# Performance work log

Hardware: AMD Instinct MI355X
Metric: run time of the kernel (lower is better)

## Reference

```python
import jax, jax.numpy as jnp
import numpy as np

NUM_LAYERS = 3
CHANNELS = 8
IN_CHANNELS = 8
MASK_OUT_STRIDE = 4
WEIGHT_NUMS = [(IN_CHANNELS + 2) * CHANNELS, CHANNELS * CHANNELS, CHANNELS]
BIAS_NUMS = [CHANNELS, CHANNELS, 1]
NUM_GEN_PARAMS = sum(WEIGHT_NUMS) + sum(BIAS_NUMS)  # 169
SOI = np.array([64.0, 128.0, 256.0, 512.0, 1024.0], dtype=np.float32)


def compute_locations(h, w, stride):
    # FCOS grid point centers, (H*W, 2) in (x, y) order
    shifts_x = jnp.arange(w, dtype=jnp.float32) * stride + stride // 2
    shifts_y = jnp.arange(h, dtype=jnp.float32) * stride + stride // 2
    ys, xs = jnp.meshgrid(shifts_y, shifts_x, indexing='ij')
    return jnp.stack([xs.reshape(-1), ys.reshape(-1)], axis=1)


def parse_dynamic_params(params):
    # params: (n_inst, 169) -> per-layer weights (n, cout, cin) and biases (n, cout)
    n = params.shape[0]
    split_pts = np.cumsum(WEIGHT_NUMS + BIAS_NUMS)[:-1].tolist()
    splits = jnp.split(params, split_pts, axis=1)
    ws, bs = [], []
    for l in range(NUM_LAYERS):
        cout = CHANNELS if l < NUM_LAYERS - 1 else 1
        ws.append(splits[l].reshape(n, cout, -1))
        bs.append(splits[NUM_LAYERS + l].reshape(n, cout))
    return ws, bs


def aligned_bilinear(x, factor):
    # Faithful port of AdelaiDet aligned_bilinear (replicate pad + align_corners=True bilinear).
    if factor == 1:
        return x
    n, c, h, w = x.shape
    xp = jnp.pad(x, ((0, 0), (0, 0), (0, 1), (0, 1)), mode='edge')  # (n,c,h+1,w+1)
    oh, ow = factor * h + 1, factor * w + 1
    # align_corners=True with oh = factor*h+1 over h+1 samples -> exact coords i/factor
    ys = jnp.arange(oh, dtype=x.dtype) / factor
    xs = jnp.arange(ow, dtype=x.dtype) / factor
    y0 = jnp.floor(ys).astype(jnp.int32)
    y1 = jnp.minimum(y0 + 1, h)
    x0 = jnp.floor(xs).astype(jnp.int32)
    x1 = jnp.minimum(x0 + 1, w)
    wy = (ys - y0.astype(x.dtype))[None, None, :, None]
    wx = (xs - x0.astype(x.dtype))[None, None, None, :]
    rows = xp[:, :, y0, :] * (1 - wy) + xp[:, :, y1, :] * wy
    out = rows[:, :, :, x0] * (1 - wx) + rows[:, :, :, x1] * wx
    pad = factor // 2
    out = jnp.pad(out, ((0, 0), (0, 0), (pad, 0), (pad, 0)), mode='edge')
    return out[:, :, :oh - 1, :ow - 1]  # (n, c, factor*h, factor*w)


def dynamic_head(x, params):
    # x: (n_inst, cin, HW); per-instance 1x1 convs == batched tiny GEMMs
    ws, bs = parse_dynamic_params(params)
    h = x
    for i, (w, b) in enumerate(zip(ws, bs)):
        h = jnp.einsum('noi,nip->nop', w, h) + b[:, :, None]
        if i < NUM_LAYERS - 1:
            h = jax.nn.relu(h)
    return h  # (n_inst, 1, HW)


def setup_inputs() -> dict:
    key = jax.random.key(0)
    k = jax.random.split(key, 6)
    N, H, W, n_inst = 2, 200, 200, 128
    return {
        'mask_feats': jax.random.normal(k[0], (N, IN_CHANNELS, H, W), jnp.float32),
        'mask_head_params': jax.random.normal(k[1], (n_inst, NUM_GEN_PARAMS), jnp.float32) * 0.1,
        'boundary_head_params': jax.random.normal(k[2], (n_inst, NUM_GEN_PARAMS), jnp.float32) * 0.1,
        'instance_locations': jax.random.uniform(k[3], (n_inst, 2), jnp.float32) * 1600.0,
        'im_inds': jax.random.randint(k[4], (n_inst,), 0, N),
        'fpn_levels': jax.random.randint(k[5], (n_inst,), 0, 5),
        'mask_feat_stride': 8,
    }


def reference(mask_feats, mask_head_params, boundary_head_params, instance_locations, im_inds, fpn_levels, mask_feat_stride):
    N, C, H, W = mask_feats.shape
    n_inst = mask_head_params.shape[0]
    locs = compute_locations(H, W, mask_feat_stride)                 # (HW, 2)
    rel = instance_locations[:, None, :] - locs[None, :, :]          # (n, HW, 2)
    rel = jnp.transpose(rel, (0, 2, 1))                              # (n, 2, HW)
    soi = jnp.asarray(SOI)[fpn_levels]                               # (n,)
    rel = (rel / soi[:, None, None]).astype(mask_feats.dtype)
    feats = mask_feats[im_inds].reshape(n_inst, C, H * W)            # per-instance gather
    x = jnp.concatenate([rel, feats], axis=1)                        # (n, C+2, HW)
    factor = mask_feat_stride // MASK_OUT_STRIDE
    m = aligned_bilinear(dynamic_head(x, mask_head_params).reshape(n_inst, 1, H, W), factor)
    bd = aligned_bilinear(dynamic_head(x, boundary_head_params).reshape(n_inst, 1, H, W), factor)
    return jax.nn.sigmoid(m), jax.nn.sigmoid(bd)
```

## Files before the change

### kernel.cpp

```cpp
#include <hip/hip_runtime.h>


#define BLOCK 256
#define Hh 200
#define Ww 200
#define NP 169
#define TH 25
#define MAXR 14
#define OW 400
#define OH 400

typedef float f32x4 __attribute__((ext_vector_type(4)));
typedef float f32x2 __attribute__((ext_vector_type(2)));
typedef _Float16 f16x4 __attribute__((ext_vector_type(4)));

__device__ __forceinline__ f32x2 splat2(float v) { f32x2 r; r.x = v; r.y = v; return r; }
__device__ __forceinline__ f32x2 pkfma(f32x2 a, f32x2 b, f32x2 c) {
    return __builtin_elementwise_fma(a, b, c);
}

__global__ __launch_bounds__(BLOCK, 4) void dmh_fused(
    const float* __restrict__ mask_feats,
    const float* __restrict__ mparams,
    const float* __restrict__ bparams,
    const float* __restrict__ ilocs,
    const int*   __restrict__ im_inds,
    const int*   __restrict__ fpn_levels,
    const int*   __restrict__ stride_p,
    float* __restrict__ out,
    int n_inst)
{
    __shared__ __align__(16) float s_par[2 * 192];
    __shared__ __align__(16) _Float16 s_m[2][MAXR][Ww];

    const int tid  = threadIdx.x;
    const int tile = blockIdx.x;
    const int inst = blockIdx.y;

    for (int j = tid; j < 2 * NP; j += BLOCK) {
        const int head = (j < NP) ? 0 : 1;
        const int k = j - head * NP;
        const float v = head ? bparams[inst * NP + k] : mparams[inst * NP + k];
        int dst;
        if      (k < 80)  dst = (k / 10) * 12 + (k % 10);
        else if (k < 144) dst = 96 + (k - 80);
        else if (k < 152) dst = 160 + (k - 144);
        else if (k < 160) dst = 168 + (k - 152);
        else if (k < 168) dst = 176 + (k - 160);
        else              dst = 184;
        s_par[head * 192 + dst] = v;
    }

    const int   s    = stride_p[0];
    const int   half = s >> 1;
    const int   im   = im_inds[inst];
    const int   lvl  = fpn_levels[inst];
    const float inv_soi = 1.0f / (float)(64 << lvl);
    const float ixl = ilocs[inst * 2 + 0];
    const float iyl = ilocs[inst * 2 + 1];

    const int i0 = tile * TH;
    const int r_begin = ((i0 > 0) ? (i0 - 1) : 0) >> 1;
    int r_end = ((i0 + TH - 2) >> 1) + 1;
    if (r_end > Hh - 1) r_end = Hh - 1;
    const int nrows = r_end - r_begin + 1;

    __syncthreads();

    const int npx = nrows * Ww;
    const float* fbase = mask_feats + (size_t)im * 8 * Hh * Ww;

    for (int g = tid * 4; g < npx; g += BLOCK * 4) {
        asm volatile("" ::: "memory");

        const int lr = g / Ww;
        const int c  = g - lr * Ww;
        const int r  = r_begin + lr;

        f32x2 xa[10], xb[10];
        {
            const float ry   = (iyl - (float)(r * s + half)) * inv_soi;
            const float step = -(float)s * inv_soi;
            const float cx0  = (ixl - (float)(c * s + half)) * inv_soi;
            xa[0].x = cx0;            xa[0].y = cx0 + step;
            xb[0].x = cx0 + 2*step;   xb[0].y = cx0 + 3*step;
            xa[1] = splat2(ry);       xb[1] = xa[1];
            const float* fp = fbase + r * Ww + c;
            #pragma unroll
            for (int ch = 0; ch < 8; ch++) {
                const f32x4 f = *(const f32x4*)(fp + ch * (Hh * Ww));
                xa[2 + ch].x = f.x; xa[2 + ch].y = f.y;
                xb[2 + ch].x = f.z; xb[2 + ch].y = f.w;
            }
        }

        #pragma unroll 1
        for (int head = 0; head < 2; head++) {
            const float* P = s_par + head * 192;
            const f32x2 zero = splat2(0.0f);

            f32x2 h1a[8], h1b[8];
            #pragma unroll
            for (int o = 0; o < 8; o++) {
                const f32x4 wa = *(const f32x4*)(P + o * 12);
                const f32x4 wb = *(const f32x4*)(P + o * 12 + 4);
                const float w8 = P[o * 12 + 8];
                const float w9 = P[o * 12 + 9];
                f32x2 aa = splat2(P[168 + o]);
                f32x2 ab = aa;
                aa = pkfma(splat2(wa.x), xa[0], aa); ab = pkfma(splat2(wa.x), xb[0], ab);
                aa = pkfma(splat2(wa.y), xa[1], aa); ab = pkfma(splat2(wa.y), xb[1], ab);
                aa = pkfma(splat2(wa.z), xa[2], aa); ab = pkfma(splat2(wa.z), xb[2], ab);
                aa = pkfma(splat2(wa.w), xa[3], aa); ab = pkfma(splat2(wa.w), xb[3], ab);
                aa = pkfma(splat2(wb.x), xa[4], aa); ab = pkfma(splat2(wb.x), xb[4], ab);
                aa = pkfma(splat2(wb.y), xa[5], aa); ab = pkfma(splat2(wb.y), xb[5], ab);
                aa = pkfma(splat2(wb.z), xa[6], aa); ab = pkfma(splat2(wb.z), xb[6], ab);
                aa = pkfma(splat2(wb.w), xa[7], aa); ab = pkfma(splat2(wb.w), xb[7], ab);
                aa = pkfma(splat2(w8),   xa[8], aa); ab = pkfma(splat2(w8),   xb[8], ab);
                aa = pkfma(splat2(w9),   xa[9], aa); ab = pkfma(splat2(w9),   xb[9], ab);
                h1a[o] = __builtin_elementwise_max(aa, zero);
                h1b[o] = __builtin_elementwise_max(ab, zero);
            }

            f32x2 h2a[8], h2b[8];
            #pragma unroll
            for (int o = 0; o < 8; o++) {
                const f32x4 wa = *(const f32x4*)(P + 96 + o * 8);
                const f32x4 wb = *(const f32x4*)(P + 96 + o * 8 + 4);
                f32x2 aa = splat2(P[176 + o]);
                f32x2 ab = aa;
                aa = pkfma(splat2(wa.x), h1a[0], aa); ab = pkfma(splat2(wa.x), h1b[0], ab);
                aa = pkfma(splat2(wa.y), h1a[1], aa); ab = pkfma(splat2(wa.y), h1b[1], ab);
                aa = pkfma(splat2(wa.z), h1a[2], aa); ab = pkfma(splat2(wa.z), h1b[2], ab);
                aa = pkfma(splat2(wa.w), h1a[3], aa); ab = pkfma(splat2(wa.w), h1b[3], ab);
                aa = pkfma(splat2(wb.x), h1a[4], aa); ab = pkfma(splat2(wb.x), h1b[4], ab);
                aa = pkfma(splat2(wb.y), h1a[5], aa); ab = pkfma(splat2(wb.y), h1b[5], ab);
                aa = pkfma(splat2(wb.z), h1a[6], aa); ab = pkfma(splat2(wb.z), h1b[6], ab);
                aa = pkfma(splat2(wb.w), h1a[7], aa); ab = pkfma(splat2(wb.w), h1b[7], ab);
                h2a[o] = __builtin_elementwise_max(aa, zero);
                h2b[o] = __builtin_elementwise_max(ab, zero);
            }

            const f32x4 wa = *(const f32x4*)(P + 160);
            const f32x4 wb = *(const f32x4*)(P + 164);
            f32x2 aa = splat2(P[184]);
            f32x2 ab = aa;
            aa = pkfma(splat2(wa.x), h2a[0], aa); ab = pkfma(splat2(wa.x), h2b[0], ab);
            aa = pkfma(splat2(wa.y), h2a[1], aa); ab = pkfma(splat2(wa.y), h2b[1], ab);
            aa = pkfma(splat2(wa.z), h2a[2], aa); ab = pkfma(splat2(wa.z), h2b[2], ab);
            aa = pkfma(splat2(wa.w), h2a[3], aa); ab = pkfma(splat2(wa.w), h2b[3], ab);
            aa = pkfma(splat2(wb.x), h2a[4], aa); ab = pkfma(splat2(wb.x), h2b[4], ab);
            aa = pkfma(splat2(wb.y), h2a[5], aa); ab = pkfma(splat2(wb.y), h2b[5], ab);
            aa = pkfma(splat2(wb.z), h2a[6], aa); ab = pkfma(splat2(wb.z), h2b[6], ab);
            aa = pkfma(splat2(wb.w), h2a[7], aa); ab = pkfma(splat2(wb.w), h2b[7], ab);

            f16x4 res;
            res.x = (_Float16)aa.x; res.y = (_Float16)aa.y;
            res.z = (_Float16)ab.x; res.w = (_Float16)ab.y;
            *(f16x4*)(&s_m[head][lr][c]) = res;
        }
    }

    __syncthreads();

    float* out0 = out + (size_t)inst * (OH * OW) + (size_t)i0 * OW;
    float* out1 = out0 + (size_t)n_inst * (OH * OW);

    const int NU = OW / 8;
    const int ntaskb = TH * NU;
    for (int t = tid; t < ntaskb; t += BLOCK) {
        const int row = t / NU;
        const int u   = t - row * NU;
        const int i   = i0 + row;
        const int ip  = (i > 0) ? (i - 1) : 0;
        const int y0  = ip >> 1;
        const float wy = (ip & 1) ? 0.5f : 0.0f;
        const int lr0 = y0 - r_begin;
        const int r1c = (y0 + 1 <= Hh - 1) ? (y0 + 1) : (Hh - 1);
        const int lr1 = r1c - r_begin;

        #pragma unroll
        for (int head = 0; head < 2; head++) {
            const f16x4 A0h = *(const f16x4*)(&s_m[head][lr0][4 * u]);
            const f16x4 A1h = *(const f16x4*)(&s_m[head][lr1][4 * u]);
            float p0 = 0.0f, p1 = 0.0f;
            if (u > 0) {
                p0 = (float)s_m[head][lr0][4 * u - 1];
                p1 = (float)s_m[head][lr1][4 * u - 1];
            }
            f32x4 B;
            B.x = (float)A0h.x + ((float)A1h.x - (float)A0h.x) * wy;
            B.y = (float)A0h.y + ((float)A1h.y - (float)A0h.y) * wy;
            B.z = (float)A0h.z + ((float)A1h.z - (float)A0h.z) * wy;
            B.w = (float)A0h.w + ((float)A1h.w - (float)A0h.w) * wy;
            const float PB = p0 + (p1 - p0) * wy;

            float o[8];
            o[0] = (u > 0) ? 0.5f * (PB + B.x) : B.x;
            o[1] = B.x;
            o[2] = 0.5f * (B.x + B.y);
            o[3] = B.y;
            o[4] = 0.5f * (B.y + B.z);
            o[5] = B.z;
            o[6] = 0.5f * (B.z + B.w);
            o[7] = B.w;

            f32x4 lo, hi;
            #pragma unroll
            for (int k = 0; k < 4; k++) lo[k] = 1.0f / (1.0f + __expf(-o[k]));
            #pragma unroll
            for (int k = 0; k < 4; k++) hi[k] = 1.0f / (1.0f + __expf(-o[4 + k]));

            float* dst = (head ? out1 : out0) + row * OW + 8 * u;
            __builtin_nontemporal_store(lo, (f32x4*)dst);
            __builtin_nontemporal_store(hi, (f32x4*)(dst + 4));
        }
    }
}

extern "C" void kernel_launch(void* const* d_in, const int* in_sizes, int n_in,
                              void* d_out, int out_size, void* d_ws, size_t ws_size,
                              hipStream_t stream) {
    const float* mask_feats = (const float*)d_in[0];
    const float* mparams    = (const float*)d_in[1];
    const float* bparams    = (const float*)d_in[2];
    const float* ilocs      = (const float*)d_in[3];
    const int*   im_inds    = (const int*)d_in[4];
    const int*   fpn_levels = (const int*)d_in[5];
    const int*   stride_p   = (const int*)d_in[6];
    float* out = (float*)d_out;

    const int n_inst = in_sizes[1] / NP;
    dim3 grid(OH / TH, n_inst);
    dim3 block(BLOCK);
    hipLaunchKernelGGL(dmh_fused, grid, block, 0, stream,
                       mask_feats, mparams, bparams, ilocs,
                       im_inds, fpn_levels, stride_p, out, n_inst);
}
```

Baseline: 73.70 us.

## Enlarge row tile and widen upsample epilogue to 16 outputs per thread

Raises the output row tile from 25 to 40, with matching halo rows, so each block covers more rows and fewer halo rows are recomputed across blocks. The upsample/sigmoid epilogue now has each thread load 8 fp16 values and emit 16 outputs through four 16-byte nontemporal stores. The sigmoid is rewritten to fold the -log2(e) scale into the interpolated values and use the hardware exp2 and rcp intrinsics. This trades a smaller grid (less parallelism) and a slightly less precise reciprocal for lower per-element ALU and instruction cost.

```diff
diff --git a/kernel.cpp b/kernel.cpp
--- a/kernel.cpp
+++ b/kernel.cpp
@@ -5,14 +5,15 @@
 #define Hh 200
 #define Ww 200
 #define NP 169
-#define TH 25
-#define MAXR 14
+#define TH 40
+#define MAXR 22
 #define OW 400
 #define OH 400
 
 typedef float f32x4 __attribute__((ext_vector_type(4)));
 typedef float f32x2 __attribute__((ext_vector_type(2)));
 typedef _Float16 f16x4 __attribute__((ext_vector_type(4)));
+typedef _Float16 f16x8 __attribute__((ext_vector_type(8)));
 
 __device__ __forceinline__ f32x2 splat2(float v) { f32x2 r; r.x = v; r.y = v; return r; }
 __device__ __forceinline__ f32x2 pkfma(f32x2 a, f32x2 b, f32x2 c) {
@@ -166,7 +167,8 @@
     float* out0 = out + (size_t)inst * (OH * OW) + (size_t)i0 * OW;
     float* out1 = out0 + (size_t)n_inst * (OH * OW);
 
-    const int NU = OW / 8;
+    const float C = -1.44269504f;
+    const int NU = OW / 16;
     const int ntaskb = TH * NU;
     for (int t = tid; t < ntaskb; t += BLOCK) {
         const int row = t / NU;
@@ -181,39 +183,46 @@
 
         #pragma unroll
         for (int head = 0; head < 2; head++) {
-            const f16x4 A0h = *(const f16x4*)(&s_m[head][lr0][4 * u]);
-            const f16x4 A1h = *(const f16x4*)(&s_m[head][lr1][4 * u]);
+            const f16x8 A0 = *(const f16x8*)(&s_m[head][lr0][8 * u]);
+            const f16x8 A1 = *(const f16x8*)(&s_m[head][lr1][8 * u]);
             float p0 = 0.0f, p1 = 0.0f;
             if (u > 0) {
-                p0 = (float)s_m[head][lr0][4 * u - 1];
-                p1 = (float)s_m[head][lr1][4 * u - 1];
-            }
-            f32x4 B;
-            B.x = (float)A0h.x + ((float)A1h.x - (float)A0h.x) * wy;
-            B.y = (float)A0h.y + ((float)A1h.y - (float)A0h.y) * wy;
-            B.z = (float)A0h.z + ((float)A1h.z - (float)A0h.z) * wy;
-            B.w = (float)A0h.w + ((float)A1h.w - (float)A0h.w) * wy;
-            const float PB = p0 + (p1 - p0) * wy;
-
-            float o[8];
-            o[0] = (u > 0) ? 0.5f * (PB + B.x) : B.x;
-            o[1] = B.x;
-            o[2] = 0.5f * (B.x + B.y);
-            o[3] = B.y;
-            o[4] = 0.5f * (B.y + B.z);
-            o[5] = B.z;
-            o[6] = 0.5f * (B.z + B.w);
-            o[7] = B.w;
-
-            f32x4 lo, hi;
-            #pragma unroll
-            for (int k = 0; k < 4; k++) lo[k] = 1.0f / (1.0f + __expf(-o[k]));
-            #pragma unroll
-            for (int k = 0; k < 4; k++) hi[k] = 1.0f / (1.0f + __expf(-o[4 + k]));
-
-            float* dst = (head ? out1 : out0) + row * OW + 8 * u;
-            __builtin_nontemporal_store(lo, (f32x4*)dst);
-            __builtin_nontemporal_store(hi, (f32x4*)(dst + 4));
+                p0 = (float)s_m[head][lr0][8 * u - 1];
+                p1 = (float)s_m[head][lr1][8 * u - 1];
+            }
+            float Bv[8];
+            #pragma unroll
+            for (int m = 0; m < 8; m++) {
+                const float a0 = (float)A0[m], a1 = (float)A1[m];
+                Bv[m] = (a0 + (a1 - a0) * wy) * C;
+            }
+            const float PB = (p0 + (p1 - p0) * wy) * C;
+
+            float e[16];
+            e[0] = (u > 0) ? 0.5f * (PB + Bv[0]) : Bv[0];
+            e[1] = Bv[0];
+            #pragma unroll
+            for (int m = 1; m < 8; m++) {
+                e[2 * m]     = 0.5f * (Bv[m - 1] + Bv[m]);
+                e[2 * m + 1] = Bv[m];
+            }
+
+            f32x4 q0, q1, q2, q3;
+            #pragma unroll
+            for (int k = 0; k < 16; k++) {
+                const float t2 = __builtin_amdgcn_exp2f(e[k]);
+                const float sg = __builtin_amdgcn_rcpf(1.0f + t2);
+                if      (k < 4)  q0[k]      = sg;
+                else if (k < 8)  q1[k - 4]  = sg;
+                else if (k < 12) q2[k - 8]  = sg;
+                else             q3[k - 12] = sg;
+            }
+
+            float* dst = (head ? out1 : out0) + row * OW + 16 * u;
+            __builtin_nontemporal_store(q0, (f32x4*)dst);
+            __builtin_nontemporal_store(q1, (f32x4*)(dst + 4));
+            __builtin_nontemporal_store(q2, (f32x4*)(dst + 8));
+            __builtin_nontemporal_store(q3, (f32x4*)(dst + 12));
         }
     }
 }
```

Result: slower. 184.7 us (+150.5%).
